# Kernel tuning notes

Measured on AMD Instinct MI355X. Metric: run time of the kernel, lower is better.

Reference implementation:

```python
import jax, jax.numpy as jnp
import numpy as np

NUM_HEADS = 16
ROPE_BASE = 10000.0


def _rope_cos_sin(seq_len, head_dim, dtype):
    inv_freq = 1.0 / (ROPE_BASE ** (jnp.arange(0, head_dim, 2, dtype=jnp.float32) / head_dim))
    t = jnp.arange(seq_len, dtype=jnp.float32)
    freqs = t[:, None] * inv_freq[None, :]          # [S, hd/2]
    emb = jnp.concatenate([freqs, freqs], axis=-1)  # [S, hd]
    return jnp.cos(emb).astype(dtype), jnp.sin(emb).astype(dtype)


def _rotate_half(x):
    x1, x2 = jnp.split(x, 2, axis=-1)
    return jnp.concatenate([-x2, x1], axis=-1)


def setup_inputs() -> dict:
    key = jax.random.key(0)
    k1, k2, k3 = jax.random.split(key, 3)
    B, S, D = 4, 2048, 1024
    x = jax.random.normal(k1, (B, S, D), dtype=jnp.float32)
    w_qkv = jax.random.normal(k2, (3 * D, D), dtype=jnp.float32) * (D ** -0.5)
    w_out = jax.random.normal(k3, (D, D), dtype=jnp.float32) * (D ** -0.5)
    return {"x": x, "w_qkv": w_qkv, "w_out": w_out}


def reference(x, w_qkv, w_out):
    B, S, D = x.shape
    H = NUM_HEADS
    hd = D // H
    scale = hd ** -0.5

    qkv = jnp.einsum('bsd,ed->bse', x, w_qkv)           # [B, S, 3D]
    qkv = qkv.reshape(B, S, 3, H, hd).transpose(2, 0, 3, 1, 4)  # [3, B, H, S, hd]
    q, k, v = qkv[0], qkv[1], qkv[2]

    cos, sin = _rope_cos_sin(S, hd, x.dtype)            # [S, hd] broadcast over B,H
    q = q * cos + _rotate_half(q) * sin
    k = k * cos + _rotate_half(k) * sin

    scores = jnp.einsum('bhqd,bhkd->bhqk', q, k) * scale  # [B, H, S, S]
    causal = jnp.tril(jnp.ones((S, S), dtype=bool))
    scores = jnp.where(causal, scores, jnp.finfo(scores.dtype).min)
    attn = jax.nn.softmax(scores, axis=-1)

    out = jnp.einsum('bhqk,bhkd->bhqd', attn, v)        # [B, H, S, hd]
    out = out.transpose(0, 2, 1, 3).reshape(B, S, D)
    out = jnp.einsum('bsd,ed->bse', out, w_out)
    return out
```

## Files before the change

### kernel.cpp

```cpp
#include <hip/hip_runtime.h>
#include <hip/hip_bf16.h>

typedef __bf16 bf16x8 __attribute__((ext_vector_type(8)));
typedef float f32x4 __attribute__((ext_vector_type(4)));
typedef __hip_bfloat16 bf16;

#define B_ 4
#define S_ 2048
#define D_ 1024
#define H_ 16
#define HD_ 64

__device__ __forceinline__ void gload16(const bf16* g, bf16* l) {
  __builtin_amdgcn_global_load_lds(
      (const __attribute__((address_space(1))) unsigned int*)g,
      (__attribute__((address_space(3))) unsigned int*)l, 16, 0, 0);
}

#define MFMA16(a, b, c) __builtin_amdgcn_mfma_f32_16x16x32_bf16((a), (b), (c), 0, 0, 0)

#define NX_ (B_ * S_ * D_)
#define NW1_ (3 * D_ * D_)
#define NW2_ (D_ * D_)
__global__ __launch_bounds__(256) void k_cvt3(const float* __restrict__ x,
                                              const float* __restrict__ w1,
                                              const float* __restrict__ w2,
                                              bf16* __restrict__ ox,
                                              bf16* __restrict__ o1,
                                              bf16* __restrict__ o2) {
  int i = (blockIdx.x * 256 + threadIdx.x) * 4;
  const float* in;
  bf16* out;
  if (i < NX_) {
    in = x; out = ox;
  } else if (i < NX_ + NW1_) {
    in = w1; out = o1; i -= NX_;
  } else {
    in = w2; out = o2; i -= NX_ + NW1_;
  }
  float4 v = *reinterpret_cast<const float4*>(in + i);
  alignas(8) bf16 t[4];
  t[0] = __float2bfloat16(v.x);
  t[1] = __float2bfloat16(v.y);
  t[2] = __float2bfloat16(v.z);
  t[3] = __float2bfloat16(v.w);
  *reinterpret_cast<uint2*>(out + i) = *reinterpret_cast<uint2*>(t);
}

__global__ __launch_bounds__(512) void k_qkv(const bf16* __restrict__ X,
                                             const bf16* __restrict__ W,
                                             bf16* __restrict__ Qw,
                                             bf16* __restrict__ Kw,
                                             bf16* __restrict__ Vtw) {
  __shared__ bf16 Al[2][128 * 64];
  __shared__ bf16 Bl[2][256 * 64];
  const int tid = threadIdx.x;
  const int wid = tid >> 6, lane = tid & 63, col = lane & 15, g = lane >> 4;
  const int wr = wid >> 2, wc = wid & 3;
  const int m0 = blockIdx.x * 128, n0 = blockIdx.y * 256;
  const int srow = tid >> 3;
  const int scol = (tid & 7) * 8;
  const int csrc = scol ^ ((srow & 7) * 8);
  const bf16* ga = X + (size_t)(m0 + srow) * 1024 + csrc;
  const bf16* gb = W + (size_t)(n0 + srow) * 1024 + csrc;
  const int ldst = srow * 64 + scol;
  const int rsw = (col & 7) * 8;
  f32x4 acc[4][4] = {};
#define QKV_STAGE_ALL(buf, k0)                               \
  do {                                                       \
    gload16(ga + (k0), &Al[buf][ldst]);                      \
    gload16(ga + (k0) + 64 * 1024, &Al[buf][ldst + 4096]);   \
    gload16(gb + (k0), &Bl[buf][ldst]);                      \
    gload16(gb + (k0) + 64 * 1024, &Bl[buf][ldst + 4096]);   \
    gload16(gb + (k0) + 128 * 1024, &Bl[buf][ldst + 8192]);  \
    gload16(gb + (k0) + 192 * 1024, &Bl[buf][ldst + 12288]); \
  } while (0)
  QKV_STAGE_ALL(0, 0);
  QKV_STAGE_ALL(1, 64);
  for (int kt = 0; kt < 16; ++kt) {
    const int c = kt & 1;
    if (kt < 15)
      asm volatile("s_waitcnt vmcnt(6)" ::: "memory");
    else
      asm volatile("s_waitcnt vmcnt(0)" ::: "memory");
    __builtin_amdgcn_s_barrier();
    const bf16* Ac = Al[c];
    const bf16* Bc = Bl[c];
    bf16x8 af[2][4], bfr[2][4];
#pragma unroll
    for (int kk = 0; kk < 2; ++kk) {
      const int ce = (kk * 32 + g * 8) ^ rsw;
#pragma unroll
      for (int m = 0; m < 4; ++m)
        af[kk][m] =
            *reinterpret_cast<const bf16x8*>(&Ac[(wr * 64 + m * 16 + col) * 64 + ce]);
#pragma unroll
      for (int n = 0; n < 4; ++n)
        bfr[kk][n] =
            *reinterpret_cast<const bf16x8*>(&Bc[(wc * 64 + n * 16 + col) * 64 + ce]);
    }
    __builtin_amdgcn_s_setprio(1);
#pragma unroll
    for (int m = 0; m < 4; ++m) {
      acc[m][0] = MFMA16(af[0][m], bfr[0][0], acc[m][0]);
      acc[m][1] = MFMA16(af[0][m], bfr[0][1], acc[m][1]);
    }
    __builtin_amdgcn_s_setprio(0);
    asm volatile("s_waitcnt lgkmcnt(0)" ::: "memory");
    __builtin_amdgcn_sched_barrier(0);
    __builtin_amdgcn_s_barrier();
    const bool more = (kt + 2 < 16);
    const int k2 = (kt + 2) * 64;
    if (more) {
      gload16(ga + k2, &Al[c][ldst]);
      gload16(ga + k2 + 64 * 1024, &Al[c][ldst + 4096]);
    }
    __builtin_amdgcn_s_setprio(1);
#pragma unroll
    for (int m = 0; m < 4; ++m) {
      acc[m][2] = MFMA16(af[0][m], bfr[0][2], acc[m][2]);
      acc[m][3] = MFMA16(af[0][m], bfr[0][3], acc[m][3]);
    }
    __builtin_amdgcn_s_setprio(0);
    if (more) {
      gload16(gb + k2, &Bl[c][ldst]);
      gload16(gb + k2 + 64 * 1024, &Bl[c][ldst + 4096]);
    }
    __builtin_amdgcn_s_setprio(1);
#pragma unroll
    for (int m = 0; m < 4; ++m) {
      acc[m][0] = MFMA16(af[1][m], bfr[1][0], acc[m][0]);
      acc[m][1] = MFMA16(af[1][m], bfr[1][1], acc[m][1]);
    }
    __builtin_amdgcn_s_setprio(0);
    if (more) {
      gload16(gb + k2 + 128 * 1024, &Bl[c][ldst + 8192]);
      gload16(gb + k2 + 192 * 1024, &Bl[c][ldst + 12288]);
    }
    __builtin_amdgcn_s_setprio(1);
#pragma unroll
    for (int m = 0; m < 4; ++m) {
      acc[m][2] = MFMA16(af[1][m], bfr[1][2], acc[m][2]);
      acc[m][3] = MFMA16(af[1][m], bfr[1][3], acc[m][3]);
    }
    __builtin_amdgcn_s_setprio(0);
  }
#undef QKV_STAGE_ALL
  const int e0 = n0 + wc * 64;
  const int which = e0 >> 10;
  const int h = (e0 >> 6) & 15;
  if (which == 2) {
#pragma unroll
    for (int m = 0; m < 4; ++m) {
      int mg = m0 + wr * 64 + m * 16 + g * 4;
      int b = mg >> 11, s = mg & 2047;
#pragma unroll
      for (int n = 0; n < 4; ++n) {
        int d = n * 16 + col;
        alignas(8) bf16 t[4];
#pragma unroll
        for (int r = 0; r < 4; ++r) t[r] = __float2bfloat16(acc[m][n][r]);
        *reinterpret_cast<uint2*>(&Vtw[((size_t)((b * 16 + h) * 64 + d) << 11) + s]) =
            *reinterpret_cast<uint2*>(t);
      }
    }
  } else {
    bf16* dst = which ? Kw : Qw;
    const float scale = which ? 1.0f : 0.18033688011112042f;
    const float fexp = -2.0f * 13.287712379549449f / 64.0f;
#pragma unroll
    for (int i = 0; i < 2; ++i) {
      int dlo = i * 16 + col;
      float invf = exp2f(fexp * (float)dlo);
#pragma unroll
      for (int m = 0; m < 4; ++m) {
        int mg = m0 + wr * 64 + m * 16 + g * 4;
        int b = mg >> 11;
        size_t rb = (size_t)(b * 16 + h) << 11;
#pragma unroll
        for (int r = 0; r < 4; ++r) {
          int s = (mg + r) & 2047;
          float sn, cs;
          __sincosf((float)s * invf, &sn, &cs);
          float lo = acc[m][i][r] * scale, hi = acc[m][i + 2][r] * scale;
          dst[((rb + s) << 6) + dlo] = __float2bfloat16(lo * cs - hi * sn);
          dst[((rb + s) << 6) + dlo + 32] = __float2bfloat16(hi * cs + lo * sn);
        }
      }
    }
  }
}

__global__ __launch_bounds__(512) void k_attn(const bf16* __restrict__ Q,
                                              const bf16* __restrict__ K,
                                              const bf16* __restrict__ Vt,
                                              bf16* __restrict__ AO) {
  __shared__ bf16 Pl[128][72];
  __shared__ bf16 Kl[2][64 * 64];
  __shared__ bf16 Vl[2][64 * 64];
  const int tid = threadIdx.x;
  const int wave = tid >> 6, lane = tid & 63, col = lane & 15, g = lane >> 4;
  const int bh = blockIdx.x;
  const size_t base = (size_t)bh << 17;
  const int r0 = tid >> 3, c0 = (tid & 7) * 8;
  const int c0s = c0 ^ ((r0 & 7) * 8);
  const int ldst = r0 * 64 + c0;
  const int swc = (col & 7) * 8;
  const int b = bh >> 4, h = bh & 15;
  const int yy = blockIdx.y, a = yy >> 2, r_ = yy & 3;
  const int qt = (a == 0) ? (15 - r_) : (a == 1) ? (8 + (r_ ^ 2)) : (a == 2) ? (4 + (r_ ^ 1)) : r_;
  const int q0 = qt * 128;
  const int qw = q0 + wave * 16;
  const int q = qw + col;
  const bf16* Qp = Q + base + (size_t)q * 64 + g * 8;
  bf16x8 qf[2];
  qf[0] = *reinterpret_cast<const bf16x8*>(Qp);
  qf[1] = *reinterpret_cast<const bf16x8*>(Qp + 32);
  const int ktlim = 2 * qt + 1;
  const int ktmax = (qw + 15) >> 6;
  const bf16* Ks = K + base + c0s;
  const bf16* Vs = Vt + base + (size_t)r0 * 2048 + c0s;
#define ATT_STAGE(buf, k0)                                  \
  do {                                                      \
    gload16(Ks + (size_t)((k0) + r0) * 64, &Kl[buf][ldst]); \
    gload16(Vs + (k0), &Vl[buf][ldst]);                     \
  } while (0)
  ATT_STAGE(0, 0);
  ATT_STAGE(1, 64);
  float l_s = 0.0f;
  f32x4 o[4] = {};
  for (int kt = 0; kt <= ktlim; ++kt) {
    const int c = kt & 1;
    const int k0 = kt * 64;
    if (kt < ktlim)
      asm volatile("s_waitcnt vmcnt(2)" ::: "memory");
    else
      asm volatile("s_waitcnt vmcnt(0)" ::: "memory");
    __builtin_amdgcn_s_barrier();
    if (kt <= ktmax) {
      const bool needmask = (k0 + 63 > qw);
      __builtin_amdgcn_s_setprio(1);
#pragma unroll
      for (int n = 0; n < 4; ++n) {
        f32x4 s = {};
#pragma unroll
        for (int kk = 0; kk < 2; ++kk) {
          bf16x8 kf = *reinterpret_cast<const bf16x8*>(
              &Kl[c][(n * 16 + col) * 64 + ((g * 8 + kk * 32) ^ swc)]);
          s = MFMA16(kf, qf[kk], s);
        }
        if (needmask) {
#pragma unroll
          for (int r = 0; r < 4; ++r)
            if (k0 + n * 16 + g * 4 + r > q) s[r] = -3e38f;
        }
        alignas(8) bf16 t[4];
#pragma unroll
        for (int r = 0; r < 4; ++r) {
          float p = exp2f(s[r]);
          l_s += p;
          t[r] = __float2bfloat16(p);
        }
        *reinterpret_cast<uint2*>(&Pl[wave * 16 + col][n * 16 + g * 4]) =
            *reinterpret_cast<uint2*>(t);
      }
#pragma unroll
      for (int kk = 0; kk < 2; ++kk) {
        bf16x8 pf =
            *reinterpret_cast<const bf16x8*>(&Pl[wave * 16 + col][g * 8 + kk * 32]);
#pragma unroll
        for (int n2 = 0; n2 < 4; ++n2) {
          bf16x8 vf = *reinterpret_cast<const bf16x8*>(
              &Vl[c][(n2 * 16 + col) * 64 + ((g * 8 + kk * 32) ^ swc)]);
          o[n2] = MFMA16(pf, vf, o[n2]);
        }
      }
      __builtin_amdgcn_s_setprio(0);
    }
    __builtin_amdgcn_s_barrier();
    if (kt + 2 <= ktlim) ATT_STAGE(c, k0 + 128);
  }
#undef ATT_STAGE
  l_s += __shfl_xor(l_s, 16);
  l_s += __shfl_xor(l_s, 32);
#pragma unroll
  for (int r = 0; r < 4; ++r) {
    float inv = 1.0f / __shfl(l_s, (lane & 48) | (g * 4 + r));
    int s = qw + g * 4 + r;
#pragma unroll
    for (int n2 = 0; n2 < 4; ++n2)
      AO[((size_t)(b * 2048 + s) << 10) + h * 64 + n2 * 16 + col] =
          __float2bfloat16(o[n2][r] * inv);
  }
}

__global__ __launch_bounds__(512) void k_outproj(const bf16* __restrict__ A,
                                                 const bf16* __restrict__ W,
                                                 float* __restrict__ OUT) {
  __shared__ bf16 Al[2][128 * 64];
  __shared__ bf16 Bl[2][256 * 64];
  const int tid = threadIdx.x;
  const int wid = tid >> 6, lane = tid & 63, col = lane & 15, g = lane >> 4;
  const int wr = wid >> 2, wc = wid & 3;
  const int m0 = blockIdx.x * 128, n0 = blockIdx.y * 256;
  const int srow = tid >> 3;
  const int scol = (tid & 7) * 8;
  const int csrc = scol ^ ((srow & 7) * 8);
  const bf16* ga = A + (size_t)(m0 + srow) * 1024 + csrc;
  const bf16* gb = W + (size_t)(n0 + srow) * 1024 + csrc;
  const int ldst = srow * 64 + scol;
  const int rsw = (col & 7) * 8;
  f32x4 acc[4][4] = {};
#define OP_STAGE_ALL(buf, k0)                                \
  do {                                                       \
    gload16(ga + (k0), &Al[buf][ldst]);                      \
    gload16(ga + (k0) + 64 * 1024, &Al[buf][ldst + 4096]);   \
    gload16(gb + (k0), &Bl[buf][ldst]);                      \
    gload16(gb + (k0) + 64 * 1024, &Bl[buf][ldst + 4096]);   \
    gload16(gb + (k0) + 128 * 1024, &Bl[buf][ldst + 8192]);  \
    gload16(gb + (k0) + 192 * 1024, &Bl[buf][ldst + 12288]); \
  } while (0)
  OP_STAGE_ALL(0, 0);
  OP_STAGE_ALL(1, 64);
  for (int kt = 0; kt < 16; ++kt) {
    const int c = kt & 1;
    if (kt < 15)
      asm volatile("s_waitcnt vmcnt(6)" ::: "memory");
    else
      asm volatile("s_waitcnt vmcnt(0)" ::: "memory");
    __builtin_amdgcn_s_barrier();
    const bf16* Ac = Al[c];
    const bf16* Bc = Bl[c];
    bf16x8 af[2][4], bfr[2][4];
#pragma unroll
    for (int kk = 0; kk < 2; ++kk) {
      const int ce = (kk * 32 + g * 8) ^ rsw;
#pragma unroll
      for (int m = 0; m < 4; ++m)
        af[kk][m] =
            *reinterpret_cast<const bf16x8*>(&Ac[(wr * 64 + m * 16 + col) * 64 + ce]);
#pragma unroll
      for (int n = 0; n < 4; ++n)
        bfr[kk][n] =
            *reinterpret_cast<const bf16x8*>(&Bc[(wc * 64 + n * 16 + col) * 64 + ce]);
    }
    __builtin_amdgcn_s_setprio(1);
#pragma unroll
    for (int m = 0; m < 4; ++m) {
      acc[m][0] = MFMA16(af[0][m], bfr[0][0], acc[m][0]);
      acc[m][1] = MFMA16(af[0][m], bfr[0][1], acc[m][1]);
    }
    __builtin_amdgcn_s_setprio(0);
    asm volatile("s_waitcnt lgkmcnt(0)" ::: "memory");
    __builtin_amdgcn_sched_barrier(0);
    __builtin_amdgcn_s_barrier();
    const bool more = (kt + 2 < 16);
    const int k2 = (kt + 2) * 64;
    if (more) {
      gload16(ga + k2, &Al[c][ldst]);
      gload16(ga + k2 + 64 * 1024, &Al[c][ldst + 4096]);
    }
    __builtin_amdgcn_s_setprio(1);
#pragma unroll
    for (int m = 0; m < 4; ++m) {
      acc[m][2] = MFMA16(af[0][m], bfr[0][2], acc[m][2]);
      acc[m][3] = MFMA16(af[0][m], bfr[0][3], acc[m][3]);
    }
    __builtin_amdgcn_s_setprio(0);
    if (more) {
      gload16(gb + k2, &Bl[c][ldst]);
      gload16(gb + k2 + 64 * 1024, &Bl[c][ldst + 4096]);
    }
    __builtin_amdgcn_s_setprio(1);
#pragma unroll
    for (int m = 0; m < 4; ++m) {
      acc[m][0] = MFMA16(af[1][m], bfr[1][0], acc[m][0]);
      acc[m][1] = MFMA16(af[1][m], bfr[1][1], acc[m][1]);
    }
    __builtin_amdgcn_s_setprio(0);
    if (more) {
      gload16(gb + k2 + 128 * 1024, &Bl[c][ldst + 8192]);
      gload16(gb + k2 + 192 * 1024, &Bl[c][ldst + 12288]);
    }
    __builtin_amdgcn_s_setprio(1);
#pragma unroll
    for (int m = 0; m < 4; ++m) {
      acc[m][2] = MFMA16(af[1][m], bfr[1][2], acc[m][2]);
      acc[m][3] = MFMA16(af[1][m], bfr[1][3], acc[m][3]);
    }
    __builtin_amdgcn_s_setprio(0);
  }
#undef OP_STAGE_ALL
#pragma unroll
  for (int m = 0; m < 4; ++m)
#pragma unroll
    for (int n = 0; n < 4; ++n)
#pragma unroll
      for (int r = 0; r < 4; ++r)
        OUT[(size_t)(m0 + wr * 64 + m * 16 + g * 4 + r) * 1024 + n0 + wc * 64 + n * 16 +
            col] = acc[m][n][r];
}

extern "C" void kernel_launch(void* const* d_in, const int* in_sizes, int n_in,
                              void* d_out, int out_size, void* d_ws, size_t ws_size,
                              hipStream_t stream) {
  const float* x = (const float*)d_in[0];
  const float* wqkv = (const float*)d_in[1];
  const float* wout = (const float*)d_in[2];
  float* out = (float*)d_out;

  char* ws = (char*)d_ws;
  const size_t SZ_X = (size_t)B_ * S_ * D_ * 2;
  const size_t SZ_WQKV = (size_t)3 * D_ * D_ * 2;
  const size_t SZ_WOUT = (size_t)D_ * D_ * 2;
  const size_t SZ_T = (size_t)B_ * H_ * S_ * HD_ * 2;
  bf16* xb = (bf16*)(ws);
  bf16* wqkvb = (bf16*)(ws + SZ_X);
  bf16* woutb = (bf16*)(ws + SZ_X + SZ_WQKV);
  bf16* qws = (bf16*)(ws + SZ_X + SZ_WQKV + SZ_WOUT);
  bf16* kws = (bf16*)(ws + SZ_X + SZ_WQKV + SZ_WOUT + SZ_T);
  bf16* vtws = (bf16*)(ws + SZ_X + SZ_WQKV + SZ_WOUT + 2 * SZ_T);
  bf16* aob = (bf16*)(ws + SZ_X + SZ_WQKV + SZ_WOUT + 3 * SZ_T);

  const int NTOT4 = (NX_ + NW1_ + NW2_) / 4;
  k_cvt3<<<NTOT4 / 256, 256, 0, stream>>>(x, wqkv, wout, xb, wqkvb, woutb);

  k_qkv<<<dim3(64, 12), 512, 0, stream>>>(xb, wqkvb, qws, kws, vtws);
  k_attn<<<dim3(B_ * H_, 16), 512, 0, stream>>>(qws, kws, vtws, aob);
  k_outproj<<<dim3(64, 4), 512, 0, stream>>>(aob, woutb, out);
}
```

Measured before the change: 159.9 us.

## Fuse fp32-to-bf16 conversion of x into the QKV GEMM A-tile load

Stops converting x to bf16 in a separate pass and instead has the QKV GEMM load fp32 x tiles into registers, convert them, and write swizzled bf16 into LDS, with a two-register-set software pipeline. This removes the standalone read and write of the 32MB fp32 activation and 16MB bf16 copy. In exchange the GEMM reads twice the A bytes from global memory (re-read across 12 column blocks), uses more registers and does VALU conversion inside the main loop, which may cost occupancy or MFMA throughput.

```diff
diff --git a/kernel.cpp b/kernel.cpp
--- a/kernel.cpp
+++ b/kernel.cpp
@@ -19,24 +19,19 @@
 
 #define MFMA16(a, b, c) __builtin_amdgcn_mfma_f32_16x16x32_bf16((a), (b), (c), 0, 0, 0)
 
-#define NX_ (B_ * S_ * D_)
 #define NW1_ (3 * D_ * D_)
 #define NW2_ (D_ * D_)
-__global__ __launch_bounds__(256) void k_cvt3(const float* __restrict__ x,
-                                              const float* __restrict__ w1,
+__global__ __launch_bounds__(256) void k_cvt2(const float* __restrict__ w1,
                                               const float* __restrict__ w2,
-                                              bf16* __restrict__ ox,
                                               bf16* __restrict__ o1,
                                               bf16* __restrict__ o2) {
   int i = (blockIdx.x * 256 + threadIdx.x) * 4;
   const float* in;
   bf16* out;
-  if (i < NX_) {
-    in = x; out = ox;
-  } else if (i < NX_ + NW1_) {
-    in = w1; out = o1; i -= NX_;
+  if (i < NW1_) {
+    in = w1; out = o1;
   } else {
-    in = w2; out = o2; i -= NX_ + NW1_;
+    in = w2; out = o2; i -= NW1_;
   }
   float4 v = *reinterpret_cast<const float4*>(in + i);
   alignas(8) bf16 t[4];
@@ -47,7 +42,7 @@
   *reinterpret_cast<uint2*>(out + i) = *reinterpret_cast<uint2*>(t);
 }
 
-__global__ __launch_bounds__(512) void k_qkv(const bf16* __restrict__ X,
+__global__ __launch_bounds__(512) void k_qkv(const float* __restrict__ Xf,
                                              const bf16* __restrict__ W,
                                              bf16* __restrict__ Qw,
                                              bf16* __restrict__ Kw,
@@ -61,91 +56,133 @@
   const int srow = tid >> 3;
   const int scol = (tid & 7) * 8;
   const int csrc = scol ^ ((srow & 7) * 8);
-  const bf16* ga = X + (size_t)(m0 + srow) * 1024 + csrc;
   const bf16* gb = W + (size_t)(n0 + srow) * 1024 + csrc;
   const int ldst = srow * 64 + scol;
+  const int ar = tid >> 2, ac4 = tid & 3;
+  const float4* gaf =
+      reinterpret_cast<const float4*>(Xf + (size_t)(m0 + ar) * 1024) + ac4 * 4;
+  const int awoff0 = ar * 64 + (((ac4 * 2 + 0) ^ (ar & 7)) * 8);
+  const int awoff1 = ar * 64 + (((ac4 * 2 + 1) ^ (ar & 7)) * 8);
   const int rsw = (col & 7) * 8;
   f32x4 acc[4][4] = {};
-#define QKV_STAGE_ALL(buf, k0)                               \
-  do {                                                       \
-    gload16(ga + (k0), &Al[buf][ldst]);                      \
-    gload16(ga + (k0) + 64 * 1024, &Al[buf][ldst + 4096]);   \
-    gload16(gb + (k0), &Bl[buf][ldst]);                      \
-    gload16(gb + (k0) + 64 * 1024, &Bl[buf][ldst + 4096]);   \
-    gload16(gb + (k0) + 128 * 1024, &Bl[buf][ldst + 8192]);  \
-    gload16(gb + (k0) + 192 * 1024, &Bl[buf][ldst + 12288]); \
-  } while (0)
-  QKV_STAGE_ALL(0, 0);
-  QKV_STAGE_ALL(1, 64);
-  for (int kt = 0; kt < 16; ++kt) {
-    const int c = kt & 1;
-    if (kt < 15)
-      asm volatile("s_waitcnt vmcnt(6)" ::: "memory");
-    else
-      asm volatile("s_waitcnt vmcnt(0)" ::: "memory");
-    __builtin_amdgcn_s_barrier();
-    const bf16* Ac = Al[c];
-    const bf16* Bc = Bl[c];
-    bf16x8 af[2][4], bfr[2][4];
-#pragma unroll
-    for (int kk = 0; kk < 2; ++kk) {
-      const int ce = (kk * 32 + g * 8) ^ rsw;
-#pragma unroll
-      for (int m = 0; m < 4; ++m)
-        af[kk][m] =
-            *reinterpret_cast<const bf16x8*>(&Ac[(wr * 64 + m * 16 + col) * 64 + ce]);
-#pragma unroll
-      for (int n = 0; n < 4; ++n)
-        bfr[kk][n] =
-            *reinterpret_cast<const bf16x8*>(&Bc[(wc * 64 + n * 16 + col) * 64 + ce]);
-    }
-    __builtin_amdgcn_s_setprio(1);
-#pragma unroll
-    for (int m = 0; m < 4; ++m) {
-      acc[m][0] = MFMA16(af[0][m], bfr[0][0], acc[m][0]);
-      acc[m][1] = MFMA16(af[0][m], bfr[0][1], acc[m][1]);
-    }
-    __builtin_amdgcn_s_setprio(0);
-    asm volatile("s_waitcnt lgkmcnt(0)" ::: "memory");
-    __builtin_amdgcn_sched_barrier(0);
-    __builtin_amdgcn_s_barrier();
-    const bool more = (kt + 2 < 16);
-    const int k2 = (kt + 2) * 64;
-    if (more) {
-      gload16(ga + k2, &Al[c][ldst]);
-      gload16(ga + k2 + 64 * 1024, &Al[c][ldst + 4096]);
-    }
-    __builtin_amdgcn_s_setprio(1);
-#pragma unroll
-    for (int m = 0; m < 4; ++m) {
-      acc[m][2] = MFMA16(af[0][m], bfr[0][2], acc[m][2]);
-      acc[m][3] = MFMA16(af[0][m], bfr[0][3], acc[m][3]);
-    }
-    __builtin_amdgcn_s_setprio(0);
-    if (more) {
-      gload16(gb + k2, &Bl[c][ldst]);
-      gload16(gb + k2 + 64 * 1024, &Bl[c][ldst + 4096]);
-    }
-    __builtin_amdgcn_s_setprio(1);
-#pragma unroll
-    for (int m = 0; m < 4; ++m) {
-      acc[m][0] = MFMA16(af[1][m], bfr[1][0], acc[m][0]);
-      acc[m][1] = MFMA16(af[1][m], bfr[1][1], acc[m][1]);
-    }
-    __builtin_amdgcn_s_setprio(0);
-    if (more) {
-      gload16(gb + k2 + 128 * 1024, &Bl[c][ldst + 8192]);
-      gload16(gb + k2 + 192 * 1024, &Bl[c][ldst + 12288]);
-    }
-    __builtin_amdgcn_s_setprio(1);
-#pragma unroll
-    for (int m = 0; m < 4; ++m) {
-      acc[m][2] = MFMA16(af[1][m], bfr[1][2], acc[m][2]);
-      acc[m][3] = MFMA16(af[1][m], bfr[1][3], acc[m][3]);
-    }
-    __builtin_amdgcn_s_setprio(0);
-  }
-#undef QKV_STAGE_ALL
+  float4 aP[4], aQ[4];
+
+#define A_LOAD(SET, KT)                               \
+  do {                                                \
+    const int kq = (KT) * 16;                         \
+    (SET)[0] = gaf[kq + 0];                           \
+    (SET)[1] = gaf[kq + 1];                           \
+    (SET)[2] = gaf[kq + 2];                           \
+    (SET)[3] = gaf[kq + 3];                           \
+  } while (0)
+#define A_CVTWRITE(SET, BUF)                          \
+  do {                                                \
+    alignas(16) bf16 t[16];                           \
+    _Pragma("unroll") for (int j = 0; j < 4; ++j) {   \
+      t[j * 4 + 0] = __float2bfloat16((SET)[j].x);    \
+      t[j * 4 + 1] = __float2bfloat16((SET)[j].y);    \
+      t[j * 4 + 2] = __float2bfloat16((SET)[j].z);    \
+      t[j * 4 + 3] = __float2bfloat16((SET)[j].w);    \
+    }                                                 \
+    *reinterpret_cast<int4*>(&Al[BUF][awoff0]) =      \
+        *reinterpret_cast<const int4*>(&t[0]);        \
+    *reinterpret_cast<int4*>(&Al[BUF][awoff1]) =      \
+        *reinterpret_cast<const int4*>(&t[8]);        \
+  } while (0)
+#define B_GLOAD_F(BUF, K0)                                     \
+  do {                                                         \
+    gload16(gb + (K0), &Bl[BUF][ldst]);                        \
+    gload16(gb + (K0) + 64 * 1024, &Bl[BUF][ldst + 4096]);     \
+  } while (0)
+#define B_GLOAD_L(BUF, K0)                                     \
+  do {                                                         \
+    gload16(gb + (K0) + 128 * 1024, &Bl[BUF][ldst + 8192]);    \
+    gload16(gb + (K0) + 192 * 1024, &Bl[BUF][ldst + 12288]);   \
+  } while (0)
+
+  A_LOAD(aQ, 0);
+  __builtin_amdgcn_sched_barrier(0);
+  B_GLOAD_F(0, 0);
+  B_GLOAD_L(0, 0);
+  __builtin_amdgcn_sched_barrier(0);
+  A_LOAD(aP, 1);
+  __builtin_amdgcn_sched_barrier(0);
+  B_GLOAD_F(1, 64);
+  B_GLOAD_L(1, 64);
+  __builtin_amdgcn_sched_barrier(0);
+  A_CVTWRITE(aQ, 0);
+
+#define QKV_BODY(KT, AWSET, ALSET)                                            \
+  {                                                                           \
+    const int c = (KT) & 1;                                                   \
+    if ((KT) < 15)                                                            \
+      asm volatile("s_waitcnt vmcnt(8) lgkmcnt(0)" ::: "memory");             \
+    else                                                                      \
+      asm volatile("s_waitcnt vmcnt(0) lgkmcnt(0)" ::: "memory");             \
+    __builtin_amdgcn_sched_barrier(0);                                        \
+    __builtin_amdgcn_s_barrier();                                             \
+    const bf16* Ac = Al[c];                                                   \
+    const bf16* Bc = Bl[c];                                                   \
+    bf16x8 af[2][4], bfr[2][4];                                               \
+    _Pragma("unroll") for (int kk = 0; kk < 2; ++kk) {                        \
+      const int ce = (kk * 32 + g * 8) ^ rsw;                                 \
+      _Pragma("unroll") for (int m = 0; m < 4; ++m) af[kk][m] =               \
+          *reinterpret_cast<const bf16x8*>(                                   \
+              &Ac[(wr * 64 + m * 16 + col) * 64 + ce]);                       \
+      _Pragma("unroll") for (int n = 0; n < 4; ++n) bfr[kk][n] =              \
+          *reinterpret_cast<const bf16x8*>(                                   \
+              &Bc[(wc * 64 + n * 16 + col) * 64 + ce]);                       \
+    }                                                                         \
+    __builtin_amdgcn_s_setprio(1);                                            \
+    _Pragma("unroll") for (int m = 0; m < 4; ++m) {                           \
+      acc[m][0] = MFMA16(af[0][m], bfr[0][0], acc[m][0]);                     \
+      acc[m][1] = MFMA16(af[0][m], bfr[0][1], acc[m][1]);                     \
+    }                                                                         \
+    __builtin_amdgcn_s_setprio(0);                                            \
+    asm volatile("s_waitcnt lgkmcnt(0)" ::: "memory");                        \
+    __builtin_amdgcn_sched_barrier(0);                                        \
+    __builtin_amdgcn_s_barrier();                                             \
+    if ((KT) + 2 < 16) {                                                      \
+      B_GLOAD_F(c, ((KT) + 2) * 64);                                          \
+      __builtin_amdgcn_sched_barrier(0);                                      \
+    }                                                                         \
+    __builtin_amdgcn_s_setprio(1);                                            \
+    _Pragma("unroll") for (int m = 0; m < 4; ++m) {                           \
+      acc[m][2] = MFMA16(af[0][m], bfr[0][2], acc[m][2]);                     \
+      acc[m][3] = MFMA16(af[0][m], bfr[0][3], acc[m][3]);                     \
+    }                                                                         \
+    __builtin_amdgcn_s_setprio(0);                                            \
+    if ((KT) + 1 < 16) { A_CVTWRITE(AWSET, c ^ 1); }                          \
+    __builtin_amdgcn_s_setprio(1);                                            \
+    _Pragma("unroll") for (int m = 0; m < 4; ++m) {                           \
+      acc[m][0] = MFMA16(af[1][m], bfr[1][0], acc[m][0]);                     \
+      acc[m][1] = MFMA16(af[1][m], bfr[1][1], acc[m][1]);                     \
+    }                                                                         \
+    __builtin_amdgcn_s_setprio(0);                                            \
+    if ((KT) + 2 < 16) {                                                      \
+      A_LOAD(ALSET, (KT) + 2);                                                \
+      __builtin_amdgcn_sched_barrier(0);                                      \
+      B_GLOAD_L(c, ((KT) + 2) * 64);                                          \
+      __builtin_amdgcn_sched_barrier(0);                                      \
+    }                                                                         \
+    __builtin_amdgcn_s_setprio(1);                                            \
+    _Pragma("unroll") for (int m = 0; m < 4; ++m) {                           \
+      acc[m][2] = MFMA16(af[1][m], bfr[1][2], acc[m][2]);                     \
+      acc[m][3] = MFMA16(af[1][m], bfr[1][3], acc[m][3]);                     \
+    }                                                                         \
+    __builtin_amdgcn_s_setprio(0);                                            \
+  }
+
+  for (int ktp = 0; ktp < 8; ++ktp) {
+    QKV_BODY(2 * ktp, aP, aQ);
+    QKV_BODY(2 * ktp + 1, aQ, aP);
+  }
+#undef QKV_BODY
+#undef A_LOAD
+#undef A_CVTWRITE
+#undef B_GLOAD_F
+#undef B_GLOAD_L
+
   const int e0 = n0 + wc * 64;
   const int which = e0 >> 10;
   const int h = (e0 >> 6) & 15;
@@ -414,7 +451,6 @@
   const size_t SZ_WQKV = (size_t)3 * D_ * D_ * 2;
   const size_t SZ_WOUT = (size_t)D_ * D_ * 2;
   const size_t SZ_T = (size_t)B_ * H_ * S_ * HD_ * 2;
-  bf16* xb = (bf16*)(ws);
   bf16* wqkvb = (bf16*)(ws + SZ_X);
   bf16* woutb = (bf16*)(ws + SZ_X + SZ_WQKV);
   bf16* qws = (bf16*)(ws + SZ_X + SZ_WQKV + SZ_WOUT);
@@ -422,10 +458,10 @@
   bf16* vtws = (bf16*)(ws + SZ_X + SZ_WQKV + SZ_WOUT + 2 * SZ_T);
   bf16* aob = (bf16*)(ws + SZ_X + SZ_WQKV + SZ_WOUT + 3 * SZ_T);
 
-  const int NTOT4 = (NX_ + NW1_ + NW2_) / 4;
-  k_cvt3<<<NTOT4 / 256, 256, 0, stream>>>(x, wqkv, wout, xb, wqkvb, woutb);
-
-  k_qkv<<<dim3(64, 12), 512, 0, stream>>>(xb, wqkvb, qws, kws, vtws);
+  const int NTOT4 = (NW1_ + NW2_) / 4;
+  k_cvt2<<<NTOT4 / 256, 256, 0, stream>>>(wqkv, wout, wqkvb, woutb);
+
+  k_qkv<<<dim3(64, 12), 512, 0, stream>>>(x, wqkvb, qws, kws, vtws);
   k_attn<<<dim3(B_ * H_, 16), 512, 0, stream>>>(qws, kws, vtws, aob);
   k_outproj<<<dim3(64, 4), 512, 0, stream>>>(aob, woutb, out);
 }
```

Measured after the change: 169.1 us. +5.8%, slower.
